# Optimization experiments

Hardware: AMD Instinct MI355X
Metric: run time of the kernel (lower is better)

## Reference

```python
import jax, jax.numpy as jnp
import numpy as np

POSE_DIM = 16
H_DIM = 32
SEQ_LEN = 25
BATCH = 262144


def setup_inputs() -> dict:
    key = jax.random.key(0)
    ks = jax.random.split(key, 9)
    s = 0.1  # keep gates out of saturation
    return {
        "first_input": jax.random.normal(ks[0], (BATCH, POSE_DIM), dtype=jnp.float32),
        "h0": jax.random.normal(ks[1], (BATCH, H_DIM), dtype=jnp.float32),
        "c0": jax.random.normal(ks[2], (BATCH, H_DIM), dtype=jnp.float32),
        # LSTM params, torch layout/gate order (i, f, g, o)
        "W_ih": s * jax.random.normal(ks[3], (4 * H_DIM, POSE_DIM), dtype=jnp.float32),
        "W_hh": s * jax.random.normal(ks[4], (4 * H_DIM, H_DIM), dtype=jnp.float32),
        "b_ih": s * jax.random.normal(ks[5], (4 * H_DIM,), dtype=jnp.float32),
        "b_hh": s * jax.random.normal(ks[6], (4 * H_DIM,), dtype=jnp.float32),
        # hidden -> input-space projection
        "W_out": s * jax.random.normal(ks[7], (POSE_DIM, H_DIM), dtype=jnp.float32),
        "b_out": s * jax.random.normal(ks[8], (POSE_DIM,), dtype=jnp.float32),
    }


def reference(first_input, h0, c0, W_ih, W_hh, b_ih, b_hh, W_out, b_out):
    # Gate order matches torch.nn.LSTM: i, f, g, o.
    b = b_ih + b_hh  # [4H]

    def step(carry, _):
        x, h, c = carry  # x: [B, P], h/c: [B, H]
        gates = x @ W_ih.T + h @ W_hh.T + b  # [B, 4H]
        i, f, g, o = jnp.split(gates, 4, axis=-1)
        c = jax.nn.sigmoid(f) * c + jax.nn.sigmoid(i) * jnp.tanh(g)
        h = jax.nn.sigmoid(o) * jnp.tanh(c)
        x_next = h @ W_out.T + b_out  # projected back to pose space [B, P]
        return (x_next, h, c), x_next

    _, preds = jax.lax.scan(step, (first_input, h0, c0), None, length=SEQ_LEN)
    # preds: [S, B, P] -> [B, S, P] to match torch cat along dim=1
    return jnp.transpose(preds, (1, 0, 2))
```

## Files before the change

### kernel.cpp

```cpp
#include <hip/hip_runtime.h>
#include <hip/hip_bf16.h>


constexpr int P = 16;
constexpr int H = 32;
constexpr int S = 25;

typedef short        bf16x8 __attribute__((ext_vector_type(8)));
typedef float        f32x16 __attribute__((ext_vector_type(16)));
typedef float        f32x4  __attribute__((ext_vector_type(4)));
typedef unsigned int u32x4  __attribute__((ext_vector_type(4)));

union FragU { u32x4 u; bf16x8 b; };

#if __has_builtin(__builtin_amdgcn_exp2f)
#define EX2 __builtin_amdgcn_exp2f
#else
#define EX2 exp2f
#endif

__device__ __forceinline__ unsigned int pkbf(float lo, float hi) {
    unsigned short a = __builtin_bit_cast(unsigned short, __float2bfloat16(lo));
    unsigned short b = __builtin_bit_cast(unsigned short, __float2bfloat16(hi));
    return (unsigned int)a | ((unsigned int)b << 16);
}

__device__ __forceinline__ float gate_scale(int r) {
    return (r >= 64 && r < 96) ? -2.8853900817779268f
                               : -1.4426950408889634f;
}

__global__ void setup_frags(const float* __restrict__ Wih, const float* __restrict__ Whh,
                            const float* __restrict__ bih, const float* __restrict__ bhh,
                            const float* __restrict__ Wout, const float* __restrict__ bout,
                            unsigned int* __restrict__ ws)
{
    auto waug = [&](int r, int k) -> float {
        float s = (r < 128) ? gate_scale(r) : 1.0f;
        if (r < 128) {
            if (k < 32) {
                float a = Whh[r * H + k];
                for (int p = 0; p < P; ++p) a += Wih[r * P + p] * Wout[p * H + k];
                return s * a;
            }
            if (k == 32) {
                float a = bih[r] + bhh[r];
                for (int p = 0; p < P; ++p) a += Wih[r * P + p] * bout[p];
                return s * a;
            }
            return 0.0f;
        } else if (r < 144) {
            int p = r - 128;
            if (k < 32)  return Wout[p * H + k];
            if (k == 32) return bout[p];
            return 0.0f;
        }
        return 0.0f;
    };
    auto w0aug = [&](int r, int k) -> float {
        float s = gate_scale(r);
        if (k < 16)  return s * Wih[r * P + k];
        if (k < 48)  return s * Whh[r * H + (k - 16)];
        if (k == 48) return s * (bih[r] + bhh[r]);
        return 0.0f;
    };

    const int tid = threadIdx.x;
    for (int idx = tid; idx < 5 * 3 * 64 * 4; idx += 256) {
        int v = idx & 3, l = (idx >> 2) & 63, tc = idx >> 8;
        int t = tc / 3, c = tc % 3;
        int r = 32 * t + (l & 31);
        int k = 16 * c + 8 * (v >> 1) + 4 * (l >> 5) + 2 * (v & 1);
        ws[idx] = pkbf(waug(r, k), waug(r, k + 1));
    }
    for (int idx = tid; idx < 4 * 4 * 64 * 4; idx += 256) {
        int v = idx & 3, l = (idx >> 2) & 63, tc = idx >> 8;
        int t = tc / 4, c = tc % 4;
        int r = 32 * t + (l & 31);
        int k = 16 * c + 8 * (v >> 1) + 4 * (l >> 5) + 2 * (v & 1);
        ws[3840 + idx] = pkbf(w0aug(r, k), w0aug(r, k + 1));
    }
}

__global__ __launch_bounds__(256, 2) void decoder_mfma(
    const float* __restrict__ x0, const float* __restrict__ h0,
    const float* __restrict__ c0, const unsigned int* __restrict__ ws,
    float* __restrict__ out, int batch)
{
    const int lane = threadIdx.x & 63;
    const int wid  = threadIdx.x >> 6;
    const int bcol = lane & 31;
    const int hi   = lane >> 5;
    const int bg   = (blockIdx.x * 4 + wid) * 32 + bcol;
    if (bg >= batch) return;

    FragU A[5][3];
    #pragma unroll
    for (int t = 0; t < 5; ++t)
        #pragma unroll
        for (int c = 0; c < 3; ++c)
            A[t][c].u = *reinterpret_cast<const u32x4*>(ws + ((t * 3 + c) * 64 + lane) * 4);

    FragU Bbias;
    Bbias.u.x = (hi == 0) ? 0x3F80u : 0u;
    Bbias.u.y = 0u; Bbias.u.z = 0u; Bbias.u.w = 0u;

    float cc[16];
    #pragma unroll
    for (int q = 0; q < 4; ++q) {
        f32x4 t = *reinterpret_cast<const f32x4*>(c0 + (size_t)bg * H + q * 8 + 4 * hi);
        cc[q * 4 + 0] = t.x; cc[q * 4 + 1] = t.y; cc[q * 4 + 2] = t.z; cc[q * 4 + 3] = t.w;
    }

    const f32x16 vzero = {};
    f32x16 acc[4];
    FragU Bh[2];

    {
        FragU B0[4];
        {
            const float* p = x0 + (size_t)bg * P;
            f32x4 a  = *reinterpret_cast<const f32x4*>(p + 4 * hi);
            f32x4 b4 = *reinterpret_cast<const f32x4*>(p + 8 + 4 * hi);
            B0[0].u.x = pkbf(a.x, a.y);  B0[0].u.y = pkbf(a.z, a.w);
            B0[0].u.z = pkbf(b4.x, b4.y); B0[0].u.w = pkbf(b4.z, b4.w);
        }
        #pragma unroll
        for (int ch = 0; ch < 2; ++ch) {
            const float* p = h0 + (size_t)bg * H + 16 * ch;
            f32x4 a  = *reinterpret_cast<const f32x4*>(p + 4 * hi);
            f32x4 b4 = *reinterpret_cast<const f32x4*>(p + 8 + 4 * hi);
            B0[1 + ch].u.x = pkbf(a.x, a.y);  B0[1 + ch].u.y = pkbf(a.z, a.w);
            B0[1 + ch].u.z = pkbf(b4.x, b4.y); B0[1 + ch].u.w = pkbf(b4.z, b4.w);
        }
        B0[3] = Bbias;

        #pragma unroll
        for (int t = 0; t < 4; ++t) acc[t] = vzero;
        #pragma unroll
        for (int c4 = 0; c4 < 4; ++c4) {
            #pragma unroll
            for (int t = 0; t < 4; ++t) {
                FragU a;
                a.u = *reinterpret_cast<const u32x4*>(ws + 3840 + ((t * 4 + c4) * 64 + lane) * 4);
                acc[t] = __builtin_amdgcn_mfma_f32_32x32x16_bf16(a.b, B0[c4].b, acc[t], 0, 0, 0);
            }
        }
    }

    auto EWPACK = [&]() {
        float hh[16];
        #pragma unroll
        for (int r = 0; r < 16; ++r) {
            const float ei = EX2(acc[0][r]);
            const float ef = EX2(acc[1][r]);
            const float eg = EX2(acc[2][r]);
            const float eo = EX2(acc[3][r]);
            const float r1 = __builtin_amdgcn_rcpf((1.0f + ei) * (1.0f + eg));
            const float tg = (1.0f - eg) * r1;
            const float rf = __builtin_amdgcn_rcpf(1.0f + ef);
            const float cn = __builtin_fmaf(cc[r], rf, tg);
            cc[r] = cn;
            const float ec = EX2(cn * -2.8853900817779268f);
            const float r2 = __builtin_amdgcn_rcpf((1.0f + ec) * (1.0f + eo));
            hh[r] = (1.0f - ec) * r2;
        }
        Bh[0].u.x = pkbf(hh[0],  hh[1]);  Bh[0].u.y = pkbf(hh[2],  hh[3]);
        Bh[0].u.z = pkbf(hh[4],  hh[5]);  Bh[0].u.w = pkbf(hh[6],  hh[7]);
        Bh[1].u.x = pkbf(hh[8],  hh[9]);  Bh[1].u.y = pkbf(hh[10], hh[11]);
        Bh[1].u.z = pkbf(hh[12], hh[13]); Bh[1].u.w = pkbf(hh[14], hh[15]);
    };
    auto PROJ = [&](f32x4& v0, f32x4& v1) {
        f32x16 px;
        px = __builtin_amdgcn_mfma_f32_32x32x16_bf16(A[4][2].b, Bbias.b, vzero, 0, 0, 0);
        px = __builtin_amdgcn_mfma_f32_32x32x16_bf16(A[4][0].b, Bh[0].b, px,    0, 0, 0);
        px = __builtin_amdgcn_mfma_f32_32x32x16_bf16(A[4][1].b, Bh[1].b, px,    0, 0, 0);
        v0 = f32x4{px[0], px[1], px[2], px[3]};
        v1 = f32x4{px[4], px[5], px[6], px[7]};
    };
    auto GATES = [&]() {
        #pragma unroll
        for (int t = 0; t < 4; ++t) {
            f32x16 a;
            a = __builtin_amdgcn_mfma_f32_32x32x16_bf16(A[t][2].b, Bbias.b, vzero, 0, 0, 0);
            a = __builtin_amdgcn_mfma_f32_32x32x16_bf16(A[t][0].b, Bh[0].b, a,    0, 0, 0);
            a = __builtin_amdgcn_mfma_f32_32x32x16_bf16(A[t][1].b, Bh[1].b, a,    0, 0, 0);
            acc[t] = a;
        }
    };

    float* const o = out + (size_t)bg * (S * P) + 4 * hi;

    f32x4 pa0, pb0, pa1, pb1, pa2, pb2, pa3, pb3;

    for (int blk = 0; blk < 6; ++blk) {
        EWPACK(); PROJ(pa0, pb0); GATES();
        EWPACK(); PROJ(pa1, pb1); GATES();
        EWPACK(); PROJ(pa2, pb2); GATES();
        EWPACK(); PROJ(pa3, pb3); GATES();
        float* ob = o + blk * 4 * P;
        *reinterpret_cast<f32x4*>(ob)              = pa0;
        *reinterpret_cast<f32x4*>(ob + 8)          = pb0;
        *reinterpret_cast<f32x4*>(ob + P)          = pa1;
        *reinterpret_cast<f32x4*>(ob + P + 8)      = pb1;
        *reinterpret_cast<f32x4*>(ob + 2 * P)      = pa2;
        *reinterpret_cast<f32x4*>(ob + 2 * P + 8)  = pb2;
        *reinterpret_cast<f32x4*>(ob + 3 * P)      = pa3;
        *reinterpret_cast<f32x4*>(ob + 3 * P + 8)  = pb3;
    }
    EWPACK();
    PROJ(pa0, pb0);
    *reinterpret_cast<f32x4*>(o + 24 * P)     = pa0;
    *reinterpret_cast<f32x4*>(o + 24 * P + 8) = pb0;
}

extern "C" void kernel_launch(void* const* d_in, const int* in_sizes, int n_in,
                              void* d_out, int out_size, void* d_ws, size_t ws_size,
                              hipStream_t stream) {
    const float* x0   = (const float*)d_in[0];
    const float* h0   = (const float*)d_in[1];
    const float* c0   = (const float*)d_in[2];
    const float* Wih  = (const float*)d_in[3];
    const float* Whh  = (const float*)d_in[4];
    const float* bih  = (const float*)d_in[5];
    const float* bhh  = (const float*)d_in[6];
    const float* Wout = (const float*)d_in[7];
    const float* bout = (const float*)d_in[8];
    float* out = (float*)d_out;
    unsigned int* ws = (unsigned int*)d_ws;

    const int batch = in_sizes[0] / P;

    hipLaunchKernelGGL(setup_frags, dim3(1), dim3(256), 0, stream,
                       Wih, Whh, bih, bhh, Wout, bout, ws);

    dim3 block(256);
    dim3 grid((batch + 127) / 128);
    hipLaunchKernelGGL(decoder_mfma, grid, block, 0, stream,
                       x0, h0, c0, ws, out, batch);
}
```

Before: 240.0 us.

## Stage output steps in LDS and write coalesced nontemporal rows

Projected outputs for 8 timesteps are buffered in a padded shared-memory tile per 128-row block, then the whole block cooperatively writes contiguous 512-byte row segments with nontemporal stores. Previously each lane issued scattered 16-byte stores strided by the 1600-byte output row. This aims to improve write coalescing and cut cache pollution, at the cost of about 66KB of LDS per block (which may limit the two-blocks-per-CU occupancy) and extra barriers. The early batch bounds check was removed, so the code assumes the batch is a multiple of 128.

```diff
diff --git a/kernel.cpp b/kernel.cpp
--- a/kernel.cpp
+++ b/kernel.cpp
@@ -5,6 +5,7 @@
 constexpr int P = 16;
 constexpr int H = 32;
 constexpr int S = 25;
+constexpr int ROWSTRIDE = 132;
 
 typedef short        bf16x8 __attribute__((ext_vector_type(8)));
 typedef float        f32x16 __attribute__((ext_vector_type(16)));
@@ -87,12 +88,14 @@
     const float* __restrict__ c0, const unsigned int* __restrict__ ws,
     float* __restrict__ out, int batch)
 {
+    __shared__ float lds[128 * ROWSTRIDE];
+
     const int lane = threadIdx.x & 63;
     const int wid  = threadIdx.x >> 6;
     const int bcol = lane & 31;
     const int hi   = lane >> 5;
-    const int bg   = (blockIdx.x * 4 + wid) * 32 + bcol;
-    if (bg >= batch) return;
+    const int rowL = wid * 32 + bcol;
+    const int bg   = blockIdx.x * 128 + rowL;
 
     FragU A[5][3];
     #pragma unroll
@@ -189,29 +192,40 @@
         }
     };
 
-    float* const o = out + (size_t)bg * (S * P) + 4 * hi;
-
-    f32x4 pa0, pb0, pa1, pb1, pa2, pb2, pa3, pb3;
-
-    for (int blk = 0; blk < 6; ++blk) {
-        EWPACK(); PROJ(pa0, pb0); GATES();
-        EWPACK(); PROJ(pa1, pb1); GATES();
-        EWPACK(); PROJ(pa2, pb2); GATES();
-        EWPACK(); PROJ(pa3, pb3); GATES();
-        float* ob = o + blk * 4 * P;
-        *reinterpret_cast<f32x4*>(ob)              = pa0;
-        *reinterpret_cast<f32x4*>(ob + 8)          = pb0;
-        *reinterpret_cast<f32x4*>(ob + P)          = pa1;
-        *reinterpret_cast<f32x4*>(ob + P + 8)      = pb1;
-        *reinterpret_cast<f32x4*>(ob + 2 * P)      = pa2;
-        *reinterpret_cast<f32x4*>(ob + 2 * P + 8)  = pb2;
-        *reinterpret_cast<f32x4*>(ob + 3 * P)      = pa3;
-        *reinterpret_cast<f32x4*>(ob + 3 * P + 8)  = pb3;
-    }
+    float* const lrow = lds + rowL * ROWSTRIDE;
+    const int blockbase = blockIdx.x * 128;
+
+    for (int c = 0; c < 3; ++c) {
+        #pragma unroll
+        for (int sl = 0; sl < 8; ++sl) {
+            EWPACK();
+            f32x4 v0, v1;
+            PROJ(v0, v1);
+            *reinterpret_cast<f32x4*>(lrow + sl * 16 + 4 * hi)     = v0;
+            *reinterpret_cast<f32x4*>(lrow + sl * 16 + 8 + 4 * hi) = v1;
+            GATES();
+        }
+        __syncthreads();
+        #pragma unroll
+        for (int k = 0; k < 16; ++k) {
+            const int u   = threadIdx.x + 256 * k;
+            const int row = u >> 5;
+            const int off = u & 31;
+            f32x4 v = *reinterpret_cast<const f32x4*>(lds + row * ROWSTRIDE + off * 4);
+            float* gp = out + (size_t)(blockbase + row) * (S * P) + c * 128 + off * 4;
+            __builtin_nontemporal_store(v, reinterpret_cast<f32x4*>(gp));
+        }
+        __syncthreads();
+    }
+
     EWPACK();
-    PROJ(pa0, pb0);
-    *reinterpret_cast<f32x4*>(o + 24 * P)     = pa0;
-    *reinterpret_cast<f32x4*>(o + 24 * P + 8) = pb0;
+    {
+        f32x4 v0, v1;
+        PROJ(v0, v1);
+        float* op = out + ((size_t)bg * S + 24) * P + 4 * hi;
+        __builtin_nontemporal_store(v0, reinterpret_cast<f32x4*>(op));
+        __builtin_nontemporal_store(v1, reinterpret_cast<f32x4*>(op + 8));
+    }
 }
 
 extern "C" void kernel_launch(void* const* d_in, const int* in_sizes, int n_in,
```

Measured after the change: 311.3 us. 29.7% more time.
